# Kernel tuning notes

Hardware: AMD Instinct MI355X
Metric: run time of the kernel (lower is better)

Reference implementation:

```python
import jax, jax.numpy as jnp
import numpy as np

# ConvVAE2d config: img_size=64, kernel=stride=16 (same-padding -> 0 pad), non-overlapping patches
BS, CH, IMG, K, NC, HID, LAT = 1024, 3, 64, 16, 10, 1024, 128
OH = IMG // K          # patches per side = 4
L = OH * OH            # patches per image = 16
PD = CH * K * K        # flattened patch dim = 768


def setup_inputs() -> dict:
    key = jax.random.key(0)
    ks = jax.random.split(key, 8)
    def w(k_, shape, fan_in):
        return jax.random.normal(k_, shape, dtype=jnp.float32) * np.float32(1.0 / np.sqrt(fan_in))
    return {
        "x": jax.random.uniform(ks[0], (BS, CH, IMG, IMG), dtype=jnp.float32),
        "c": jax.random.uniform(ks[1], (BS, NC), dtype=jnp.float32),
        # cvae_small.encode params: [patch++class] -> hidden -> 2*latent
        "enc_w1": w(ks[2], (PD + NC, HID), PD + NC),
        "enc_b1": jnp.zeros((HID,), jnp.float32),
        "enc_w2": w(ks[3], (HID, 2 * LAT), HID),
        "enc_b2": jnp.zeros((2 * LAT,), jnp.float32),
        # cvae_small.decode params: [z++class] -> hidden -> patch (sigmoid)
        "dec_w1": w(ks[4], (LAT + NC, HID), LAT + NC),
        "dec_b1": jnp.zeros((HID,), jnp.float32),
        "dec_w2": w(ks[5], (HID, PD), HID),
        "dec_b2": jnp.zeros((PD,), jnp.float32),
    }


def reference(x, c, enc_w1, enc_b1, enc_w2, enc_b2, dec_w1, dec_b1, dec_w2, dec_b2):
    bs = x.shape[0]
    # --- encode_vae_layer: unfold into [bs, L, ch*k*k] patches (stride=k, pad=0) ---
    p = x.reshape(bs, CH, OH, K, OH, K).transpose(0, 2, 4, 1, 3, 5).reshape(bs, L, PD)
    cb = jnp.broadcast_to(c[:, None, :], (bs, L, NC))  # class vector per patch
    h = jax.nn.relu(jnp.concatenate([p, cb], axis=-1) @ enc_w1 + enc_b1)
    mu_logvar = h @ enc_w2 + enc_b2                    # [bs, L, 2*LAT]
    # --- reparameterize_vae_layer (deterministic=True -> z = mu) ---
    mu = mu_logvar[..., :LAT]
    # --- decode_vae_layer: per-patch decode, then fold back (non-overlapping) ---
    hd = jax.nn.relu(jnp.concatenate([mu, cb], axis=-1) @ dec_w1 + dec_b1)
    patches = jax.nn.sigmoid(hd @ dec_w2 + dec_b2)     # [bs, L, PD]
    recon = (patches.reshape(bs, OH, OH, CH, K, K)
                     .transpose(0, 3, 1, 4, 2, 5)
                     .reshape(bs, CH, IMG, IMG))
    # mu_logvar as a [bs, 2*latent, h/stride, w/stride] feature map
    mu_logvar_2d = mu_logvar.transpose(0, 2, 1).reshape(bs, 2 * LAT, OH, OH)
    return recon, mu_logvar_2d
```

## Files before the change

kernel.cpp:

```cpp
#include <hip/hip_runtime.h>

typedef unsigned short u16;
typedef unsigned int   u32;
typedef __bf16 bf16x8 __attribute__((ext_vector_type(8)));
typedef float  f32x4  __attribute__((ext_vector_type(4)));

__device__ __forceinline__ u16 f2b(float f) {
  u32 u = __builtin_bit_cast(u32, f);
  u = (u + 0x7fffu + ((u >> 16) & 1u)) >> 16;
  return (u16)u;
}
__device__ __forceinline__ float b2f(u16 h) {
  u32 u = ((u32)h) << 16;
  return __builtin_bit_cast(float, u);
}
__device__ __forceinline__ float ld_in(const void* p, size_t idx, int isf32) {
  return isf32 ? ((const float*)p)[idx] : b2f(((const u16*)p)[idx]);
}
__device__ __forceinline__ void async_cp16(const u16* g, u16* l) {
  __builtin_amdgcn_global_load_lds(
      (const __attribute__((address_space(1))) void*)g,
      (__attribute__((address_space(3))) void*)l, 16, 0, 0);
}

#define RECON_ELEMS 12582912

__global__ __launch_bounds__(256) void detect_f32(const u16* __restrict__ x,
                                                  int* __restrict__ flag) {
  __shared__ int s;
  if (threadIdx.x == 0) s = 0;
  __syncthreads();
  int bad = 0;
  for (int i = threadIdx.x; i < 2048; i += 256) {
    u16 u = x[i];
    if ((u & 0x8000u) || (u > 0x3F80u)) bad = 1;
  }
  if (bad) atomicOr(&s, 1);
  __syncthreads();
  if (threadIdx.x == 0) *flag = s;
}

__global__ __launch_bounds__(256) void build_a1(const void* __restrict__ x,
                                                const void* __restrict__ c,
                                                u16* __restrict__ A1,
                                                int R, int rowOff,
                                                const int* __restrict__ flag) {
  int g = blockIdx.x * 256 + threadIdx.x;
  if (g >= R * 112) return;
  int row = g / 112, grp = g - row * 112;
  int grow = row + rowOff;
  int b = grow >> 4, l = grow & 15, oh = l >> 2, ow = l & 3;
  int isf = *flag;
  u16* dst = &A1[(size_t)row * 896 + grp * 8];
  int col0 = grp * 8;
  if (col0 < 768) {
    int ch = col0 >> 8, kh = (col0 >> 4) & 15, kw = col0 & 15;
    size_t off = (size_t)b * 12288 + ch * 4096 + (oh * 16 + kh) * 64 + ow * 16 + kw;
    if (isf) {
      const float* s = (const float*)x + off;
      float4 f0 = *(const float4*)(s);
      float4 f1 = *(const float4*)(s + 4);
      dst[0] = f2b(f0.x); dst[1] = f2b(f0.y); dst[2] = f2b(f0.z); dst[3] = f2b(f0.w);
      dst[4] = f2b(f1.x); dst[5] = f2b(f1.y); dst[6] = f2b(f1.z); dst[7] = f2b(f1.w);
    } else {
      *(int4*)dst = *(const int4*)((const u16*)x + off);
    }
  } else {
#pragma unroll
    for (int t = 0; t < 8; ++t) {
      int col = col0 + t;
      dst[t] = (col < 778) ? f2b(ld_in(c, (size_t)b * 10 + (col - 768), isf)) : (u16)0;
    }
  }
}

__global__ __launch_bounds__(256) void prep_weights(const void* __restrict__ ew1,
                                                    const void* __restrict__ ew2,
                                                    const void* __restrict__ dw1,
                                                    const void* __restrict__ dw2,
                                                    u16* __restrict__ W1t,
                                                    u16* __restrict__ EW2t,
                                                    u16* __restrict__ W3t,
                                                    u16* __restrict__ DW2t,
                                                    const int* __restrict__ flag) {
  const int z = blockIdx.z;
  const void* src; u16* dst; int N, Kpad, Ksrc;
  if (z == 0)      { src = ew1; dst = W1t;  N = 1024; Kpad = 896;  Ksrc = 778;  }
  else if (z == 1) { src = ew2; dst = EW2t; N = 256;  Kpad = 1024; Ksrc = 1024; }
  else if (z == 2) { src = dw1; dst = W3t;  N = 1024; Kpad = 160;  Ksrc = 138;  }
  else             { src = dw2; dst = DW2t; N = 768;  Kpad = 1024; Ksrc = 1024; }
  const int k0 = blockIdx.x * 32, n0 = blockIdx.y * 32;
  if (k0 >= Kpad || n0 >= N) return;
  __shared__ float t[32][33];
  const int tx = threadIdx.x & 31, ty = threadIdx.x >> 5;
  const int isf = *flag;
#pragma unroll
  for (int j = 0; j < 4; ++j) {
    int k = k0 + ty + j * 8;
    t[ty + j * 8][tx] = (k < Ksrc) ? ld_in(src, (size_t)k * N + n0 + tx, isf) : 0.0f;
  }
  __syncthreads();
#pragma unroll
  for (int j = 0; j < 4; ++j) {
    int n = n0 + ty + j * 8;
    dst[(size_t)n * Kpad + k0 + tx] = f2b(t[tx][ty + j * 8]);
  }
}

__global__ __launch_bounds__(256) void build_a3_tail(const void* __restrict__ c,
                                                     u16* __restrict__ A3,
                                                     int R, int rowOff,
                                                     const int* __restrict__ flag) {
  int i = blockIdx.x * 256 + threadIdx.x;
  if (i >= R * 32) return;
  int row = i >> 5, col = 128 + (i & 31);
  int b = (row + rowOff) >> 4;
  int isf = *flag;
  A3[(size_t)row * 160 + col] = (col < 138) ? f2b(ld_in(c, (size_t)b * 10 + col - 128, isf)) : (u16)0;
}

template <int EPI>
__global__ __launch_bounds__(256, 3) void gemm_k(const u16* __restrict__ A,
                                                 const u16* __restrict__ Bt,
                                                 const void* __restrict__ bias,
                                                 u16* __restrict__ outb,
                                                 float* __restrict__ outf,
                                                 u16* __restrict__ out1,
                                                 int N, int K, int GY, int rowOff,
                                                 const int* __restrict__ flag) {
  __shared__ __align__(16) u16 As[2][128 * 32];
  __shared__ __align__(16) u16 Bs[2][128 * 32];
  const int bid = blockIdx.x;
  const int by = bid % GY, bx = bid / GY;
  const int rowBase = by * 128, colBase = bx * 128;
  const int tid  = threadIdx.x;
  const int lane = tid & 63;
  const int wave = tid >> 6;
  const int wr = (wave >> 1) * 64, wc = (wave & 1) * 64;
  const int quad = lane >> 4, l16 = lane & 15;
  const int swq = quad ^ ((l16 >> 1) & 3);

  const int isf = *flag;
  float bv[4];
#pragma unroll
  for (int j = 0; j < 4; ++j) bv[j] = ld_in(bias, colBase + wc + j * 16 + l16, isf);
  asm volatile("s_waitcnt vmcnt(0)" ::: "memory");

  const int s0 = tid, s1 = 256 + tid;
  const int r0 = s0 >> 2, q0 = (s0 & 3) ^ ((s0 >> 3) & 3);
  const int r1 = s1 >> 2, q1 = (s1 & 3) ^ ((s1 >> 3) & 3);
  const u16* gA0 = &A[(size_t)(rowBase + r0) * K + q0 * 8];
  const u16* gA1 = &A[(size_t)(rowBase + r1) * K + q1 * 8];
  const u16* gB0 = &Bt[(size_t)(colBase + r0) * K + q0 * 8];
  const u16* gB1 = &Bt[(size_t)(colBase + r1) * K + q1 * 8];

  f32x4 acc[4][4] = {};
  const int NI = K >> 5;

  async_cp16(gA0, &As[0][s0 * 8]);
  async_cp16(gA1, &As[0][s1 * 8]);
  async_cp16(gB0, &Bs[0][s0 * 8]);
  async_cp16(gB1, &Bs[0][s1 * 8]);

  int p = 0;
  for (int it = 0; it < NI; ++it) {
    if (it + 1 < NI) {
      const int kn = (it + 1) << 5;
      const int np = p ^ 1;
      async_cp16(gA0 + kn, &As[np][s0 * 8]);
      async_cp16(gA1 + kn, &As[np][s1 * 8]);
      async_cp16(gB0 + kn, &Bs[np][s0 * 8]);
      async_cp16(gB1 + kn, &Bs[np][s1 * 8]);
      asm volatile("s_waitcnt vmcnt(4)\n\ts_barrier" ::: "memory");
    } else {
      asm volatile("s_waitcnt vmcnt(0)\n\ts_barrier" ::: "memory");
    }
    const u16* Ap = As[p];
    const u16* Bp = Bs[p];
    bf16x8 af[4], bfr[4];
#pragma unroll
    for (int i = 0; i < 4; ++i)
      af[i] = *(const bf16x8*)(&Ap[(wr + i * 16 + l16) * 32 + swq * 8]);
#pragma unroll
    for (int j = 0; j < 4; ++j)
      bfr[j] = *(const bf16x8*)(&Bp[(wc + j * 16 + l16) * 32 + swq * 8]);
#pragma unroll
    for (int i = 0; i < 4; ++i)
#pragma unroll
      for (int j = 0; j < 4; ++j)
        acc[i][j] = __builtin_amdgcn_mfma_f32_16x16x32_bf16(af[i], bfr[j], acc[i][j], 0, 0, 0);
    asm volatile("s_waitcnt lgkmcnt(0)\n\ts_barrier" ::: "memory");
    p ^= 1;
  }

#pragma unroll
  for (int i = 0; i < 4; ++i) {
    int row0 = rowBase + wr + i * 16 + quad * 4;
#pragma unroll
    for (int j = 0; j < 4; ++j) {
      int col = colBase + wc + j * 16 + l16;
#pragma unroll
      for (int r = 0; r < 4; ++r) {
        int row = row0 + r;
        int grow = row + rowOff;
        float v = acc[i][j][r] + bv[j];
        if (EPI == 0) {
          v = fmaxf(v, 0.0f);
          outb[(size_t)row * N + col] = f2b(v);
        } else {
          int b = grow >> 4, lr = grow & 15;
          outf[(size_t)b * 4096 + col * 16 + lr] = v;
          if (col < 128) out1[(size_t)row * 160 + col] = f2b(v);
        }
      }
    }
  }
}

template <int EPI>
__global__ __launch_bounds__(512, 2) void gemm_r3(const u16* __restrict__ A,
                                                  const u16* __restrict__ Bt,
                                                  const void* __restrict__ bias,
                                                  u16* __restrict__ outb,
                                                  float* __restrict__ outf,
                                                  int N, int K, int NBX, int NBY,
                                                  int rowOff,
                                                  const int* __restrict__ flag) {
  extern __shared__ __align__(16) u16 lds[];
  const int bid = blockIdx.x;
  const int xcd = bid & 7, idx = bid >> 3;
  const int byl = idx / NBX;
  const int by = xcd * (NBY >> 3) + byl;
  const int bx = idx - byl * NBX;
  const int rowBase = by * 256, colBase = bx * 256;

  const int tid = threadIdx.x;
  const int lane = tid & 63, w = tid >> 6;
  const int l16 = lane & 15, quad = lane >> 4;
  const int wm = w >> 2, wn = w & 3;
  const int swq = quad ^ ((l16 >> 1) & 3);

  const int isf = *flag;
  float bv[4];
#pragma unroll
  for (int nr = 0; nr < 4; ++nr)
    bv[nr] = ld_in(bias, colBase + wn * 64 + nr * 16 + l16, isf);
  asm volatile("s_waitcnt vmcnt(0)" ::: "memory");

  const int sA0 = tid, sA1 = tid + 512;
  const int rA0 = sA0 >> 2, qA0 = (sA0 & 3) ^ ((rA0 >> 1) & 3);
  const int rA1 = sA1 >> 2, qA1 = (sA1 & 3) ^ ((rA1 >> 1) & 3);
  const u16* gA0 = A  + (size_t)(rowBase + rA0) * K + qA0 * 8;
  const u16* gA1 = A  + (size_t)(rowBase + rA1) * K + qA1 * 8;
  const u16* gB0 = Bt + (size_t)(colBase + rA0) * K + qA0 * 8;
  const u16* gB1 = Bt + (size_t)(colBase + rA1) * K + qA1 * 8;

  f32x4 acc[8][4] = {};
  bf16x8 a[8], b[4];
  const int NT = K >> 5;

  async_cp16(gA0, lds + tid * 8);
  async_cp16(gA1, lds + 4096 + tid * 8);
  async_cp16(gB0, lds + 8192 + tid * 8);
  async_cp16(gB1, lds + 12288 + tid * 8);
  if (NT > 1) {
    u16* D = lds + 16384;
    async_cp16(gA0 + 32, D + tid * 8);
    async_cp16(gA1 + 32, D + 4096 + tid * 8);
    async_cp16(gB0 + 32, D + 8192 + tid * 8);
    async_cp16(gB1 + 32, D + 12288 + tid * 8);
    asm volatile("s_waitcnt vmcnt(4)" ::: "memory");
  } else {
    asm volatile("s_waitcnt vmcnt(0)" ::: "memory");
  }
  __builtin_amdgcn_s_barrier();

  int cur = 0;
  for (int t = 0; t < NT; ++t) {
    const u16* Lq = lds + cur * 16384;
#pragma unroll
    for (int mr = 0; mr < 8; ++mr)
      a[mr] = *(const bf16x8*)(Lq + (wm * 128 + mr * 16 + l16) * 32 + swq * 8);
#pragma unroll
    for (int nr = 0; nr < 4; ++nr)
      b[nr] = *(const bf16x8*)(Lq + 8192 + (wn * 64 + nr * 16 + l16) * 32 + swq * 8);
    if (t + 2 < NT) {
      const int d2 = (cur >= 1) ? cur - 1 : 2;
      u16* D = lds + d2 * 16384;
      const int ko = (t + 2) * 32;
      async_cp16(gA0 + ko, D + tid * 8);
      async_cp16(gA1 + ko, D + 4096 + tid * 8);
      async_cp16(gB0 + ko, D + 8192 + tid * 8);
      async_cp16(gB1 + ko, D + 12288 + tid * 8);
    }
    asm volatile("s_waitcnt lgkmcnt(0)" ::: "memory");
    __builtin_amdgcn_sched_barrier(0);
    __builtin_amdgcn_s_setprio(1);
#pragma unroll
    for (int mr = 0; mr < 8; ++mr)
#pragma unroll
      for (int nr = 0; nr < 4; ++nr)
        acc[mr][nr] = __builtin_amdgcn_mfma_f32_16x16x32_bf16(a[mr], b[nr], acc[mr][nr], 0, 0, 0);
    __builtin_amdgcn_s_setprio(0);
    __builtin_amdgcn_sched_barrier(0);
    if (t + 2 < NT)      asm volatile("s_waitcnt vmcnt(4)" ::: "memory");
    else if (t + 1 < NT) asm volatile("s_waitcnt vmcnt(0)" ::: "memory");
    if (t + 1 < NT) __builtin_amdgcn_s_barrier();
    cur = (cur >= 2) ? 0 : cur + 1;
  }

#pragma unroll
  for (int mr = 0; mr < 8; ++mr) {
    const int row0 = rowBase + wm * 128 + mr * 16 + quad * 4;
#pragma unroll
    for (int nr = 0; nr < 4; ++nr) {
      const int col = colBase + wn * 64 + nr * 16 + l16;
#pragma unroll
      for (int r = 0; r < 4; ++r) {
        const int row = row0 + r;
        float v = acc[mr][nr][r] + bv[nr];
        if (EPI == 0) {
          v = fmaxf(v, 0.0f);
          outb[(size_t)row * N + col] = f2b(v);
        } else {
          v = 1.0f / (1.0f + __expf(-v));
          const int grow = row + rowOff;
          const int bb = grow >> 4, l = grow & 15;
          const int oh = l >> 2, ow = l & 3;
          const int ch = col >> 8, kh = (col >> 4) & 15, kw = col & 15;
          outf[(size_t)bb * 12288 + ch * 4096 + (oh * 16 + kh) * 64 + ow * 16 + kw] = v;
        }
      }
    }
  }
}


extern "C" void kernel_launch(void* const* d_in, const int* in_sizes, int n_in,
                              void* d_out, int out_size, void* d_ws, size_t ws_size,
                              hipStream_t stream) {
  const void* x   = d_in[0];
  const void* c   = d_in[1];
  const void* ew1 = d_in[2];
  const void* eb1 = d_in[3];
  const void* ew2 = d_in[4];
  const void* eb2 = d_in[5];
  const void* dw1 = d_in[6];
  const void* db1 = d_in[7];
  const void* dw2 = d_in[8];
  const void* db2 = d_in[9];
  float* out  = (float*)d_out;
  u16*   ws   = (u16*)d_ws;

  static bool configured = false;
  if (!configured) {
    hipFuncSetAttribute(reinterpret_cast<const void*>(gemm_r3<0>),
                        hipFuncAttributeMaxDynamicSharedMemorySize, 98304);
    hipFuncSetAttribute(reinterpret_cast<const void*>(gemm_r3<2>),
                        hipFuncAttributeMaxDynamicSharedMemorySize, 98304);
    configured = true;
  }

  const size_t fixedU16 = 8 + 917504 + 262144 + 163840 + 786432;
  int R = 2048;
  for (int cand = 16384; cand >= 2048; cand >>= 1) {
    if ((fixedU16 + (size_t)cand * 2080) * 2 <= ws_size) { R = cand; break; }
  }

  int* flag = (int*)ws;
  u16* W1t  = ws + 8;
  u16* EW2t = W1t + 917504;
  u16* W3t  = EW2t + 262144;
  u16* DW2t = W3t + 163840;
  u16* A1c  = DW2t + 786432;
  u16* hc   = A1c + (size_t)R * 896;
  u16* A3c  = hc + (size_t)R * 1024;
  float* out2 = out + RECON_ELEMS;

  detect_f32<<<dim3(1), dim3(256), 0, stream>>>((const u16*)x, flag);

  prep_weights<<<dim3(32, 32, 4), dim3(256), 0, stream>>>(ew1, ew2, dw1, dw2,
                                                          W1t, EW2t, W3t, DW2t, flag);

  const int chunks = 16384 / R;
  const int GY  = R / 128;
  const int NBY = R / 256;
  for (int chunk = 0; chunk < chunks; ++chunk) {
    int rowOff = chunk * R;
    build_a1<<<dim3((R * 112 + 255) / 256), dim3(256), 0, stream>>>(x, c, A1c, R, rowOff, flag);
    build_a3_tail<<<dim3((R * 32) / 256), dim3(256), 0, stream>>>(c, A3c, R, rowOff, flag);
    gemm_r3<0><<<dim3(4 * NBY), dim3(512), 98304, stream>>>(A1c, W1t, eb1, hc, nullptr,
                                                            1024, 896, 4, NBY, rowOff, flag);
    gemm_k<1><<<dim3(2 * GY), dim3(256), 0, stream>>>(hc, EW2t, eb2, nullptr, out2, A3c, 256, 1024, GY, rowOff, flag);
    gemm_k<0><<<dim3(8 * GY), dim3(256), 0, stream>>>(A3c, W3t, db1, hc, nullptr, nullptr, 1024, 160, GY, rowOff, flag);
    gemm_r3<2><<<dim3(3 * NBY), dim3(512), 98304, stream>>>(hc, DW2t, db2, nullptr, out,
                                                            768, 1024, 3, NBY, rowOff, flag);
  }
}
```

Before: 267.8 us.

## Fuse encoder-second and decoder-first GEMMs into one row-block kernel

Replaces the build_a3_tail kernel and the two gemm_k launches with one gemm_mid kernel. Each block owns 64 rows: it computes mu_logvar, writes it out, assembles the decoder input (mu plus class vector) in LDS, then runs the decoder first layer and writes the hidden activations back in place into the same buffer. This removes two launches and the global round trip of the A3 intermediate. The cost is less parallelism per chunk (R/64 blocks), large LDS use that limits occupancy, and a full 256-wide EW2 tile reloaded per block.

```diff
diff --git a/kernel.cpp b/kernel.cpp
--- a/kernel.cpp
+++ b/kernel.cpp
@@ -107,116 +107,6 @@
   }
 }
 
-__global__ __launch_bounds__(256) void build_a3_tail(const void* __restrict__ c,
-                                                     u16* __restrict__ A3,
-                                                     int R, int rowOff,
-                                                     const int* __restrict__ flag) {
-  int i = blockIdx.x * 256 + threadIdx.x;
-  if (i >= R * 32) return;
-  int row = i >> 5, col = 128 + (i & 31);
-  int b = (row + rowOff) >> 4;
-  int isf = *flag;
-  A3[(size_t)row * 160 + col] = (col < 138) ? f2b(ld_in(c, (size_t)b * 10 + col - 128, isf)) : (u16)0;
-}
-
-template <int EPI>
-__global__ __launch_bounds__(256, 3) void gemm_k(const u16* __restrict__ A,
-                                                 const u16* __restrict__ Bt,
-                                                 const void* __restrict__ bias,
-                                                 u16* __restrict__ outb,
-                                                 float* __restrict__ outf,
-                                                 u16* __restrict__ out1,
-                                                 int N, int K, int GY, int rowOff,
-                                                 const int* __restrict__ flag) {
-  __shared__ __align__(16) u16 As[2][128 * 32];
-  __shared__ __align__(16) u16 Bs[2][128 * 32];
-  const int bid = blockIdx.x;
-  const int by = bid % GY, bx = bid / GY;
-  const int rowBase = by * 128, colBase = bx * 128;
-  const int tid  = threadIdx.x;
-  const int lane = tid & 63;
-  const int wave = tid >> 6;
-  const int wr = (wave >> 1) * 64, wc = (wave & 1) * 64;
-  const int quad = lane >> 4, l16 = lane & 15;
-  const int swq = quad ^ ((l16 >> 1) & 3);
-
-  const int isf = *flag;
-  float bv[4];
-#pragma unroll
-  for (int j = 0; j < 4; ++j) bv[j] = ld_in(bias, colBase + wc + j * 16 + l16, isf);
-  asm volatile("s_waitcnt vmcnt(0)" ::: "memory");
-
-  const int s0 = tid, s1 = 256 + tid;
-  const int r0 = s0 >> 2, q0 = (s0 & 3) ^ ((s0 >> 3) & 3);
-  const int r1 = s1 >> 2, q1 = (s1 & 3) ^ ((s1 >> 3) & 3);
-  const u16* gA0 = &A[(size_t)(rowBase + r0) * K + q0 * 8];
-  const u16* gA1 = &A[(size_t)(rowBase + r1) * K + q1 * 8];
-  const u16* gB0 = &Bt[(size_t)(colBase + r0) * K + q0 * 8];
-  const u16* gB1 = &Bt[(size_t)(colBase + r1) * K + q1 * 8];
-
-  f32x4 acc[4][4] = {};
-  const int NI = K >> 5;
-
-  async_cp16(gA0, &As[0][s0 * 8]);
-  async_cp16(gA1, &As[0][s1 * 8]);
-  async_cp16(gB0, &Bs[0][s0 * 8]);
-  async_cp16(gB1, &Bs[0][s1 * 8]);
-
-  int p = 0;
-  for (int it = 0; it < NI; ++it) {
-    if (it + 1 < NI) {
-      const int kn = (it + 1) << 5;
-      const int np = p ^ 1;
-      async_cp16(gA0 + kn, &As[np][s0 * 8]);
-      async_cp16(gA1 + kn, &As[np][s1 * 8]);
-      async_cp16(gB0 + kn, &Bs[np][s0 * 8]);
-      async_cp16(gB1 + kn, &Bs[np][s1 * 8]);
-      asm volatile("s_waitcnt vmcnt(4)\n\ts_barrier" ::: "memory");
-    } else {
-      asm volatile("s_waitcnt vmcnt(0)\n\ts_barrier" ::: "memory");
-    }
-    const u16* Ap = As[p];
-    const u16* Bp = Bs[p];
-    bf16x8 af[4], bfr[4];
-#pragma unroll
-    for (int i = 0; i < 4; ++i)
-      af[i] = *(const bf16x8*)(&Ap[(wr + i * 16 + l16) * 32 + swq * 8]);
-#pragma unroll
-    for (int j = 0; j < 4; ++j)
-      bfr[j] = *(const bf16x8*)(&Bp[(wc + j * 16 + l16) * 32 + swq * 8]);
-#pragma unroll
-    for (int i = 0; i < 4; ++i)
-#pragma unroll
-      for (int j = 0; j < 4; ++j)
-        acc[i][j] = __builtin_amdgcn_mfma_f32_16x16x32_bf16(af[i], bfr[j], acc[i][j], 0, 0, 0);
-    asm volatile("s_waitcnt lgkmcnt(0)\n\ts_barrier" ::: "memory");
-    p ^= 1;
-  }
-
-#pragma unroll
-  for (int i = 0; i < 4; ++i) {
-    int row0 = rowBase + wr + i * 16 + quad * 4;
-#pragma unroll
-    for (int j = 0; j < 4; ++j) {
-      int col = colBase + wc + j * 16 + l16;
-#pragma unroll
-      for (int r = 0; r < 4; ++r) {
-        int row = row0 + r;
-        int grow = row + rowOff;
-        float v = acc[i][j][r] + bv[j];
-        if (EPI == 0) {
-          v = fmaxf(v, 0.0f);
-          outb[(size_t)row * N + col] = f2b(v);
-        } else {
-          int b = grow >> 4, lr = grow & 15;
-          outf[(size_t)b * 4096 + col * 16 + lr] = v;
-          if (col < 128) out1[(size_t)row * 160 + col] = f2b(v);
-        }
-      }
-    }
-  }
-}
-
 template <int EPI>
 __global__ __launch_bounds__(512, 2) void gemm_r3(const u16* __restrict__ A,
                                                   const u16* __restrict__ Bt,
@@ -335,6 +225,180 @@
   }
 }
 
+__global__ __launch_bounds__(512, 2) void gemm_mid(u16* hio,
+    const u16* __restrict__ EW2t, const u16* __restrict__ W3t,
+    const void* __restrict__ c, const void* __restrict__ eb2,
+    const void* __restrict__ db1, float* __restrict__ out2,
+    int rowOff, const int* __restrict__ flag) {
+  extern __shared__ __align__(16) u16 lds[];
+  const int bid = blockIdx.x;
+  const int lrowBase = bid * 64;
+  const int growBase = rowOff + lrowBase;
+  const int tid = threadIdx.x;
+  const int lane = tid & 63, w = tid >> 6;
+  const int l16 = lane & 15, quad = lane >> 4;
+  const int swq = quad ^ ((l16 >> 1) & 3);
+  const int wm = w >> 2, wn4 = w & 3;
+
+  const int isf = *flag;
+  float bv2[2], bv3[8][2];
+#pragma unroll
+  for (int nr = 0; nr < 2; ++nr)
+    bv2[nr] = ld_in(eb2, w * 32 + nr * 16 + l16, isf);
+#pragma unroll
+  for (int np = 0; np < 8; ++np)
+#pragma unroll
+    for (int nr = 0; nr < 2; ++nr)
+      bv3[np][nr] = ld_in(db1, np * 128 + wn4 * 32 + nr * 16 + l16, isf);
+  asm volatile("s_waitcnt vmcnt(0)" ::: "memory");
+
+  const int rA = tid >> 3, rcA = tid & 7;
+  const int gcA = (rcA & 4) | ((rcA & 3) ^ ((rA >> 1) & 3));
+  const u16* gAe = hio + (size_t)(lrowBase + rA) * 1024 + gcA * 8;
+  const u16* gBe[4];
+#pragma unroll
+  for (int j = 0; j < 4; ++j) {
+    const int sb = tid + j * 512;
+    const int rB = sb >> 3, rcB = sb & 7;
+    const int gcB = (rcB & 4) | ((rcB & 3) ^ ((rB >> 1) & 3));
+    gBe[j] = EW2t + (size_t)rB * 1024 + gcB * 8;
+  }
+
+#define STGE(tt, s) do {                                                   \
+    async_cp16(gAe + (tt) * 64, lds + (s) * 4096 + tid * 8);               \
+    _Pragma("unroll") for (int j = 0; j < 4; ++j)                          \
+      async_cp16(gBe[j] + (tt) * 64,                                       \
+                 lds + 8192 + (s) * 16384 + (tid + j * 512) * 8);          \
+  } while (0)
+
+  f32x4 acce[4][2] = {};
+  STGE(0, 0);
+  int p = 0;
+  for (int t = 0; t < 16; ++t) {
+    if (t + 1 < 16) {
+      STGE(t + 1, p ^ 1);
+      asm volatile("s_waitcnt vmcnt(5)\n\ts_barrier" ::: "memory");
+    } else {
+      asm volatile("s_waitcnt vmcnt(0)\n\ts_barrier" ::: "memory");
+    }
+    const u16* AE = lds + p * 4096;
+    const u16* BE = lds + 8192 + p * 16384;
+    bf16x8 ae[4][2], be[2][2];
+#pragma unroll
+    for (int mr = 0; mr < 4; ++mr)
+#pragma unroll
+      for (int ks = 0; ks < 2; ++ks)
+        ae[mr][ks] = *(const bf16x8*)(AE + (mr * 16 + l16) * 64 + ((ks * 4) | swq) * 8);
+#pragma unroll
+    for (int nr = 0; nr < 2; ++nr)
+#pragma unroll
+      for (int ks = 0; ks < 2; ++ks)
+        be[nr][ks] = *(const bf16x8*)(BE + (w * 32 + nr * 16 + l16) * 64 + ((ks * 4) | swq) * 8);
+    asm volatile("s_waitcnt lgkmcnt(0)" ::: "memory");
+    __builtin_amdgcn_sched_barrier(0);
+    __builtin_amdgcn_s_setprio(1);
+#pragma unroll
+    for (int mr = 0; mr < 4; ++mr)
+#pragma unroll
+      for (int nr = 0; nr < 2; ++nr)
+#pragma unroll
+        for (int ks = 0; ks < 2; ++ks)
+          acce[mr][nr] = __builtin_amdgcn_mfma_f32_16x16x32_bf16(ae[mr][ks], be[nr][ks], acce[mr][nr], 0, 0, 0);
+    __builtin_amdgcn_s_setprio(0);
+    __builtin_amdgcn_sched_barrier(0);
+    __builtin_amdgcn_s_barrier();
+    p ^= 1;
+  }
+#undef STGE
+
+  u16* A3 = lds + 40960;
+#pragma unroll
+  for (int mr = 0; mr < 4; ++mr)
+#pragma unroll
+    for (int nr = 0; nr < 2; ++nr) {
+      const int col = w * 32 + nr * 16 + l16;
+      const int row0 = mr * 16 + quad * 4;
+#pragma unroll
+      for (int r = 0; r < 4; ++r) {
+        const int row = row0 + r;
+        const int grow = growBase + row;
+        const float v = acce[mr][nr][r] + bv2[nr];
+        out2[(size_t)(grow >> 4) * 4096 + col * 16 + (grow & 15)] = v;
+        if (col < 128) A3[row * 168 + col] = f2b(v);
+      }
+    }
+  {
+    const int rT = tid >> 3, cg = tid & 7;
+    const int b = (growBase + rT) >> 4;
+#pragma unroll
+    for (int jj = 0; jj < 5; ++jj) {
+      const int col = 128 + cg * 5 + jj;
+      A3[rT * 168 + col] = (col < 138) ? f2b(ld_in(c, (size_t)b * 10 + col - 128, isf)) : (u16)0;
+    }
+  }
+  asm volatile("s_waitcnt vmcnt(0) lgkmcnt(0)" ::: "memory");
+  __builtin_amdgcn_s_barrier();
+
+  int nW[5], cW[5];
+#pragma unroll
+  for (int j = 0; j < 5; ++j) {
+    const int s5 = tid + j * 512;
+    nW[j] = s5 / 20;
+    cW[j] = s5 - nW[j] * 20;
+  }
+#pragma unroll
+  for (int j = 0; j < 5; ++j)
+    async_cp16(W3t + (size_t)nW[j] * 160 + cW[j] * 8, lds + (tid + j * 512) * 8);
+  asm volatile("s_waitcnt vmcnt(0)" ::: "memory");
+  __builtin_amdgcn_s_barrier();
+
+  for (int np = 0; np < 8; ++np) {
+    const int pb = np & 1;
+    if (np < 7) {
+#pragma unroll
+      for (int j = 0; j < 5; ++j)
+        async_cp16(W3t + (size_t)((np + 1) * 128 + nW[j]) * 160 + cW[j] * 8,
+                   lds + (pb ^ 1) * 20480 + (tid + j * 512) * 8);
+    }
+    f32x4 accd[2][2] = {};
+    const u16* WP = lds + pb * 20480;
+#pragma unroll
+    for (int t = 0; t < 5; ++t) {
+      bf16x8 ad[2], bd[2];
+#pragma unroll
+      for (int mr = 0; mr < 2; ++mr)
+        ad[mr] = *(const bf16x8*)(A3 + (wm * 32 + mr * 16 + l16) * 168 + (t * 4 + quad) * 8);
+#pragma unroll
+      for (int nr = 0; nr < 2; ++nr)
+        bd[nr] = *(const bf16x8*)(WP + (wn4 * 32 + nr * 16 + l16) * 160 + (t * 4 + quad) * 8);
+      asm volatile("s_waitcnt lgkmcnt(0)" ::: "memory");
+      __builtin_amdgcn_sched_barrier(0);
+#pragma unroll
+      for (int mr = 0; mr < 2; ++mr)
+#pragma unroll
+        for (int nr = 0; nr < 2; ++nr)
+          accd[mr][nr] = __builtin_amdgcn_mfma_f32_16x16x32_bf16(ad[mr], bd[nr], accd[mr][nr], 0, 0, 0);
+    }
+#pragma unroll
+    for (int mr = 0; mr < 2; ++mr)
+#pragma unroll
+      for (int nr = 0; nr < 2; ++nr) {
+        const int col = np * 128 + wn4 * 32 + nr * 16 + l16;
+        const int row0 = wm * 32 + mr * 16 + quad * 4;
+#pragma unroll
+        for (int r = 0; r < 4; ++r) {
+          const int row = row0 + r;
+          const float v = fmaxf(accd[mr][nr][r] + bv3[np][nr], 0.0f);
+          hio[(size_t)(lrowBase + row) * 1024 + col] = f2b(v);
+        }
+      }
+    if (np < 7) {
+      asm volatile("s_waitcnt vmcnt(16)" ::: "memory");
+      __builtin_amdgcn_s_barrier();
+    }
+  }
+}
+
 
 extern "C" void kernel_launch(void* const* d_in, const int* in_sizes, int n_in,
                               void* d_out, int out_size, void* d_ws, size_t ws_size,
@@ -358,13 +422,15 @@
                         hipFuncAttributeMaxDynamicSharedMemorySize, 98304);
     hipFuncSetAttribute(reinterpret_cast<const void*>(gemm_r3<2>),
                         hipFuncAttributeMaxDynamicSharedMemorySize, 98304);
+    hipFuncSetAttribute(reinterpret_cast<const void*>(gemm_mid),
+                        hipFuncAttributeMaxDynamicSharedMemorySize, 103424);
     configured = true;
   }
 
   const size_t fixedU16 = 8 + 917504 + 262144 + 163840 + 786432;
   int R = 2048;
   for (int cand = 16384; cand >= 2048; cand >>= 1) {
-    if ((fixedU16 + (size_t)cand * 2080) * 2 <= ws_size) { R = cand; break; }
+    if ((fixedU16 + (size_t)cand * 1920) * 2 <= ws_size) { R = cand; break; }
   }
 
   int* flag = (int*)ws;
@@ -374,7 +440,6 @@
   u16* DW2t = W3t + 163840;
   u16* A1c  = DW2t + 786432;
   u16* hc   = A1c + (size_t)R * 896;
-  u16* A3c  = hc + (size_t)R * 1024;
   float* out2 = out + RECON_ELEMS;
 
   detect_f32<<<dim3(1), dim3(256), 0, stream>>>((const u16*)x, flag);
@@ -383,16 +448,14 @@
                                                           W1t, EW2t, W3t, DW2t, flag);
 
   const int chunks = 16384 / R;
-  const int GY  = R / 128;
   const int NBY = R / 256;
   for (int chunk = 0; chunk < chunks; ++chunk) {
     int rowOff = chunk * R;
     build_a1<<<dim3((R * 112 + 255) / 256), dim3(256), 0, stream>>>(x, c, A1c, R, rowOff, flag);
-    build_a3_tail<<<dim3((R * 32) / 256), dim3(256), 0, stream>>>(c, A3c, R, rowOff, flag);
     gemm_r3<0><<<dim3(4 * NBY), dim3(512), 98304, stream>>>(A1c, W1t, eb1, hc, nullptr,
                                                             1024, 896, 4, NBY, rowOff, flag);
-    gemm_k<1><<<dim3(2 * GY), dim3(256), 0, stream>>>(hc, EW2t, eb2, nullptr, out2, A3c, 256, 1024, GY, rowOff, flag);
-    gemm_k<0><<<dim3(8 * GY), dim3(256), 0, stream>>>(A3c, W3t, db1, hc, nullptr, nullptr, 1024, 160, GY, rowOff, flag);
+    gemm_mid<<<dim3(R / 64), dim3(512), 103424, stream>>>(hc, EW2t, W3t, c, eb2, db1,
+                                                          out2, rowOff, flag);
     gemm_r3<2><<<dim3(3 * NBY), dim3(512), 98304, stream>>>(hc, DW2t, db2, nullptr, out,
                                                             768, 1024, 3, NBY, rowOff, flag);
   }
```

Result: faster. 244.9 us (-8.5%).
